# Kernel optimization log

Measured on AMD Instinct MI355X. Metric: run time of the kernel, lower is better.

## Reference

```python
import jax, jax.numpy as jnp
import numpy as np

K = 16          # filter order (number of Laplacian powers)
MLP_OUT = 16    # mlp_hid == mlp_out for mlp_nlayers == 1
D_PE = 64       # phi output dim
BN_EPS = 1e-5
B, N, M = 8, 1024, 128
E = 131072


def setup_inputs() -> dict:
    key = jax.random.key(0)
    ks = jax.random.split(key, 12)
    # Symmetric, spectrally-bounded Laplacian surrogate so 15 matrix powers stay finite.
    A = jax.random.normal(ks[0], (B, N, N), dtype=jnp.float32)
    Lap = (A + jnp.swapaxes(A, -1, -2)) * (0.5 / jnp.sqrt(jnp.float32(N)))
    W = jax.random.normal(ks[1], (B, N, M), dtype=jnp.float32)
    edge_index = jax.random.randint(ks[2], (2, E), 0, B * N, dtype=jnp.int64)
    batch = jnp.repeat(jnp.arange(B, dtype=jnp.int64), N)
    # MLP layer (k -> MLP_OUT) + BatchNorm affine params
    lin_w = jax.random.normal(ks[3], (K, MLP_OUT), dtype=jnp.float32) / jnp.sqrt(jnp.float32(K))
    lin_b = jnp.zeros((MLP_OUT,), dtype=jnp.float32)
    bn_gamma = jnp.ones((MLP_OUT,), dtype=jnp.float32)
    bn_beta = jnp.zeros((MLP_OUT,), dtype=jnp.float32)
    # phi: GIN-style 2-layer MLP after neighbor aggregation
    phi_w1 = jax.random.normal(ks[4], (MLP_OUT, D_PE), dtype=jnp.float32) / jnp.sqrt(jnp.float32(MLP_OUT))
    phi_b1 = jnp.zeros((D_PE,), dtype=jnp.float32)
    phi_w2 = jax.random.normal(ks[5], (D_PE, D_PE), dtype=jnp.float32) / jnp.sqrt(jnp.float32(D_PE))
    phi_b2 = jnp.zeros((D_PE,), dtype=jnp.float32)
    return {"Lap": Lap, "W": W, "lin_w": lin_w, "lin_b": lin_b,
            "bn_gamma": bn_gamma, "bn_beta": bn_beta,
            "phi_w1": phi_w1, "phi_b1": phi_b1, "phi_w2": phi_w2, "phi_b2": phi_b2,
            "edge_index": edge_index, "batch": batch}


def _filter(S, W0):
    """Sequential power filter: returns [k, N, M] = [W0, S@W0, S^2@W0, ...]."""
    def step(out, _):
        nxt = S @ out
        return nxt, nxt
    _, rest = jax.lax.scan(step, W0, None, length=K - 1)
    return jnp.concatenate([W0[None], rest], axis=0)


def reference(Lap, W, lin_w, lin_b, bn_gamma, bn_beta,
              phi_w1, phi_b1, phi_w2, phi_b2, edge_index, batch):
    # Batched filter over all graphs: [B, k, N, M] -> [B, N, M, k]
    feat = jax.vmap(_filter)(Lap, W)
    feat = jnp.transpose(feat, (0, 2, 3, 1))
    # Linear over k -> MLP_OUT channels: [B, N, M, C]
    h = feat @ lin_w + lin_b
    # BatchNorm1d (training mode), per-graph statistics over (N, M) per channel,
    # matching the torch per-graph loop where BN sees [M, C, N].
    mean = jnp.mean(h, axis=(1, 2), keepdims=True)
    var = jnp.var(h, axis=(1, 2), keepdims=True)
    h = (h - mean) * jax.lax.rsqrt(var + BN_EPS) * bn_gamma + bn_beta
    h = jax.nn.relu(h)
    # phi: pool random-sample dim M, flatten graphs -> [N_sum, C]
    x = jnp.mean(h, axis=2).reshape(-1, h.shape[-1])
    src, dst = edge_index[0], edge_index[1]
    agg = jax.ops.segment_sum(x[src], dst, num_segments=x.shape[0])
    g = x + agg  # GIN aggregation
    out = jax.nn.relu(g @ phi_w1 + phi_b1) @ phi_w2 + phi_b2  # [N_sum, D_PE]
    return out
```

## Files before the change

### kernel.cpp

```cpp
#include <hip/hip_runtime.h>

#define B 8
#define N 1024
#define M 128
#define KF 16
#define C 16
#define DPE 64
#define NE 131072
#define NV (B*N)
#define NM (N*M)
#define BN_EPS 1e-5f

typedef short bf16x8 __attribute__((ext_vector_type(8)));
typedef float f32x4 __attribute__((ext_vector_type(4)));

__device__ inline unsigned short f2bf_rne(float f) {
    unsigned u = __float_as_uint(f);
    u += 0x7fffu + ((u >> 16) & 1u);
    return (unsigned short)(u >> 16);
}
__device__ inline float bf2f(unsigned short s) {
    return __uint_as_float((unsigned)s << 16);
}
__device__ inline void split_bf16(float v, unsigned short& hi, unsigned short& lo) {
    hi = f2bf_rne(v);
    float hf = __uint_as_float((unsigned)hi << 16);
    lo = f2bf_rne(v - hf);
}
union U4 { uint4 v; unsigned short s[8]; };
union U2 { uint2 v; unsigned short s[4]; };

__device__ __host__ inline size_t PF4(int b, int msub, int ks, int hl, int l) {
    return ((((size_t)b * 8 + msub) * 32 + ks) * 2 + hl) * 64 + l;
}
#define PFBUF ((size_t)B * 8 * 32 * 2 * 64)

__global__ __launch_bounds__(256) void prep_all(const float* __restrict__ W,
                                                const int* __restrict__ ei,
                                                uint4* __restrict__ Pf,
                                                unsigned short* __restrict__ feat,
                                                int* __restrict__ cnt) {
    __shared__ float T[32][33];
    int blk = blockIdx.x;
    int t = threadIdx.x;
    if (blk < 1024) {
        int b = blk & 7;
        int tile = blk >> 3;
        int nt = tile & 31, mt = tile >> 5;
        int n0 = nt * 32, m0 = mt * 32;
        {
            int nl = t >> 3, mq = t & 7;
            float4 v = *(const float4*)(W + ((size_t)b * N + n0 + nl) * M + m0 + mq * 4);
            T[nl][mq * 4 + 0] = v.x; T[nl][mq * 4 + 1] = v.y;
            T[nl][mq * 4 + 2] = v.z; T[nl][mq * 4 + 3] = v.w;
        }
        __syncthreads();
        {
            int ml = t >> 3, nq = t & 7;
            U2 o;
            o.s[0] = f2bf_rne(T[nq * 4 + 0][ml]);
            o.s[1] = f2bf_rne(T[nq * 4 + 1][ml]);
            o.s[2] = f2bf_rne(T[nq * 4 + 2][ml]);
            o.s[3] = f2bf_rne(T[nq * 4 + 3][ml]);
            unsigned short* plane = feat + (size_t)b * KF * NM;
            *(uint2*)(plane + (size_t)(m0 + ml) * N + n0 + nq * 4) = o.v;
        }
        if (t < 128) {
            int unit = t >> 6, l = t & 63;
            int msub = 2 * mt + unit;
            U4 hi, lo;
            #pragma unroll
            for (int j = 0; j < 8; j++) {
                float v = T[8 * (l >> 4) + j][16 * unit + (l & 15)];
                split_bf16(v, hi.s[j], lo.s[j]);
            }
            Pf[PF4(b, msub, nt, 0, l)] = hi.v;
            Pf[PF4(b, msub, nt, 1, l)] = lo.v;
        }
    } else {
        int e = (blk - 1024) * 256 + t;
        bool is64 = (ei[1] == 0 && ei[3] == 0 && ei[5] == 0 && ei[7] == 0);
        int dst = is64 ? ei[2 * (NE + e)] : ei[NE + e];
        atomicAdd(&cnt[dst], 1);
    }
}

__global__ __launch_bounds__(512) void gemm_chain(const float* __restrict__ Lap,
                                                  uint4* __restrict__ PfA,
                                                  uint4* __restrict__ PfB,
                                                  unsigned short* __restrict__ feat,
                                                  unsigned* bar) {
    extern __shared__ __align__(16) char smem[];
    uint4* ldsS = (uint4*)smem;
    float* Dl = (float*)(smem + 131072);

    int b = blockIdx.x & 7, bx = blockIdx.x >> 3;
    int t = threadIdx.x;
    int w = t >> 6, lane = t & 63;
    int g = w >> 2, wq = w & 3;
    int n0 = 32 * bx;

    {
        int nl = (lane & 15) + 16 * (t >> 8);
        int kg = (lane >> 4) + 4 * ((t >> 6) & 3);
        const float* row = Lap + ((size_t)b * N + n0 + nl) * N;
        int base = (t >> 8) * 4096;
        #pragma unroll
        for (int jj = 0; jj < 8; jj++) {
            int koct = kg + 16 * jj;
            int k0 = koct * 8;
            float4 f0 = *(const float4*)(row + k0);
            float4 f1 = *(const float4*)(row + k0 + 4);
            float e[8] = {f0.x, f0.y, f0.z, f0.w, f1.x, f1.y, f1.z, f1.w};
            U4 hi, lo;
            #pragma unroll
            for (int j = 0; j < 8; j++) split_bf16(e[j], hi.s[j], lo.s[j]);
            int ks = koct >> 2;
            int l = (nl & 15) + 16 * (koct & 3);
            ldsS[base + ks * 128 + l] = hi.v;
            ldsS[base + ks * 128 + 64 + l] = lo.v;
        }
    }
    __syncthreads();

    #pragma unroll 1
    for (int k = 0; k < KF - 1; k++) {
        const uint4* PfIn = (k & 1) ? PfB : PfA;
        uint4* PfOut      = (k & 1) ? PfA : PfB;
        const uint4* Pw0 = PfIn + (size_t)(b * 8 + 2 * wq) * 4096 + (size_t)(16 * g) * 128;
        const uint4* Pw1 = Pw0 + 4096;

        f32x4 acc[2][2] = {};
        uint4 ph[2][2], pl[2][2];
        #pragma unroll
        for (int q = 0; q < 2; q++) {
            ph[q][0] = Pw0[(size_t)q * 128 + lane];
            pl[q][0] = Pw0[(size_t)q * 128 + 64 + lane];
            ph[q][1] = Pw1[(size_t)q * 128 + lane];
            pl[q][1] = Pw1[(size_t)q * 128 + 64 + lane];
        }
        #pragma unroll 2
        for (int ks = 0; ks < 16; ks++) {
            int kg = 16 * g + ks;
            uint4 a0h = ph[ks & 1][0], a0l = pl[ks & 1][0];
            uint4 a1h = ph[ks & 1][1], a1l = pl[ks & 1][1];
            if (ks < 14) {
                ph[ks & 1][0] = Pw0[(size_t)(ks + 2) * 128 + lane];
                pl[ks & 1][0] = Pw0[(size_t)(ks + 2) * 128 + 64 + lane];
                ph[ks & 1][1] = Pw1[(size_t)(ks + 2) * 128 + lane];
                pl[ks & 1][1] = Pw1[(size_t)(ks + 2) * 128 + 64 + lane];
            }
            bf16x8 b0h = __builtin_bit_cast(bf16x8, ldsS[kg * 128 + lane]);
            bf16x8 b0l = __builtin_bit_cast(bf16x8, ldsS[kg * 128 + 64 + lane]);
            bf16x8 b1h = __builtin_bit_cast(bf16x8, ldsS[4096 + kg * 128 + lane]);
            bf16x8 b1l = __builtin_bit_cast(bf16x8, ldsS[4096 + kg * 128 + 64 + lane]);
            bf16x8 A0h = __builtin_bit_cast(bf16x8, a0h);
            bf16x8 A0l = __builtin_bit_cast(bf16x8, a0l);
            bf16x8 A1h = __builtin_bit_cast(bf16x8, a1h);
            bf16x8 A1l = __builtin_bit_cast(bf16x8, a1l);
            acc[0][0] = __builtin_amdgcn_mfma_f32_16x16x32_bf16(A0h, b0h, acc[0][0], 0, 0, 0);
            acc[0][0] = __builtin_amdgcn_mfma_f32_16x16x32_bf16(A0h, b0l, acc[0][0], 0, 0, 0);
            acc[0][0] = __builtin_amdgcn_mfma_f32_16x16x32_bf16(A0l, b0h, acc[0][0], 0, 0, 0);
            acc[0][1] = __builtin_amdgcn_mfma_f32_16x16x32_bf16(A0h, b1h, acc[0][1], 0, 0, 0);
            acc[0][1] = __builtin_amdgcn_mfma_f32_16x16x32_bf16(A0h, b1l, acc[0][1], 0, 0, 0);
            acc[0][1] = __builtin_amdgcn_mfma_f32_16x16x32_bf16(A0l, b1h, acc[0][1], 0, 0, 0);
            acc[1][0] = __builtin_amdgcn_mfma_f32_16x16x32_bf16(A1h, b0h, acc[1][0], 0, 0, 0);
            acc[1][0] = __builtin_amdgcn_mfma_f32_16x16x32_bf16(A1h, b0l, acc[1][0], 0, 0, 0);
            acc[1][0] = __builtin_amdgcn_mfma_f32_16x16x32_bf16(A1l, b0h, acc[1][0], 0, 0, 0);
            acc[1][1] = __builtin_amdgcn_mfma_f32_16x16x32_bf16(A1h, b1h, acc[1][1], 0, 0, 0);
            acc[1][1] = __builtin_amdgcn_mfma_f32_16x16x32_bf16(A1h, b1l, acc[1][1], 0, 0, 0);
            acc[1][1] = __builtin_amdgcn_mfma_f32_16x16x32_bf16(A1l, b1h, acc[1][1], 0, 0, 0);
        }

        if (g == 1) {
            #pragma unroll
            for (int mi = 0; mi < 2; mi++)
                #pragma unroll
                for (int ni = 0; ni < 2; ni++)
                    #pragma unroll
                    for (int r = 0; r < 4; r++) {
                        int m = 32 * wq + 16 * mi + 4 * (lane >> 4) + r;
                        int c = 16 * ni + (lane & 15);
                        Dl[m * 36 + c] = acc[mi][ni][r];
                    }
        }
        __syncthreads();
        if (g == 0) {
            #pragma unroll
            for (int mi = 0; mi < 2; mi++)
                #pragma unroll
                for (int ni = 0; ni < 2; ni++)
                    #pragma unroll
                    for (int r = 0; r < 4; r++) {
                        int m = 32 * wq + 16 * mi + 4 * (lane >> 4) + r;
                        int c = 16 * ni + (lane & 15);
                        Dl[m * 36 + c] += acc[mi][ni][r];
                    }
        }
        __syncthreads();

        {
            int m = t >> 2, c0 = (t & 3) * 8;
            float4 v0 = *(const float4*)&Dl[m * 36 + c0];
            float4 v1 = *(const float4*)&Dl[m * 36 + c0 + 4];
            float e[8] = {v0.x, v0.y, v0.z, v0.w, v1.x, v1.y, v1.z, v1.w};
            U4 hi, lo;
            #pragma unroll
            for (int j = 0; j < 8; j++) split_bf16(e[j], hi.s[j], lo.s[j]);
            unsigned short* plane = feat + ((size_t)b * KF + (k + 1)) * NM
                                        + (size_t)m * N + n0 + c0;
            *(uint4*)plane = hi.v;
            if (k < KF - 2) {
                int l = (m & 15) + 16 * (c0 >> 3);
                PfOut[PF4(b, m >> 4, bx, 0, l)] = hi.v;
                PfOut[PF4(b, m >> 4, bx, 1, l)] = lo.v;
            }
        }
        if (k < KF - 2) {
            __syncthreads();
            if (t == 0) {
                __hip_atomic_fetch_add(&bar[b * 32], 1u, __ATOMIC_RELAXED,
                                       __HIP_MEMORY_SCOPE_AGENT);
                unsigned target = 32u * (unsigned)(k + 1);
                while (__hip_atomic_load(&bar[b * 32], __ATOMIC_RELAXED,
                                         __HIP_MEMORY_SCOPE_AGENT) < target)
                    __builtin_amdgcn_s_sleep(1);
            }
            __syncthreads();
            asm volatile("buffer_inv sc0\n\ts_waitcnt vmcnt(0)" ::: "memory");
        }
    }
}

__global__ __launch_bounds__(256) void bn_stats_scan(const unsigned short* __restrict__ feat,
                                                     const float* __restrict__ lin_w,
                                                     const float* __restrict__ lin_b,
                                                     float* __restrict__ stats,
                                                     const int* __restrict__ cnt,
                                                     int* __restrict__ off,
                                                     int* __restrict__ cur) {
    __shared__ float wls[KF * C];
    __shared__ float red[4][2][C];
    __shared__ int ss[256];
    int t = threadIdx.x;
    if (blockIdx.x < 8) {
        if (blockIdx.x == 0) {
            int base = t * 32;
            int local[32];
            int s = 0;
            #pragma unroll
            for (int i = 0; i < 32; i++) { local[i] = cnt[base + i]; s += local[i]; }
            ss[t] = s;
            __syncthreads();
            #pragma unroll
            for (int d = 1; d < 256; d <<= 1) {
                int v = (t >= d) ? ss[t - d] : 0;
                __syncthreads();
                ss[t] += v;
                __syncthreads();
            }
            int excl = ss[t] - s;
            #pragma unroll
            for (int i = 0; i < 32; i++) { off[base + i] = excl; cur[base + i] = excl; excl += local[i]; }
        }
        return;
    }
    int blk = blockIdx.x - 8;
    wls[t] = lin_w[t];
    __syncthreads();
    int b = blk & 7;
    int i = (blk >> 3) * 256 + t;
    const uint2* fb = (const uint2*)(feat + (size_t)b * KF * NM);

    float4 hacc[C];
    #pragma unroll
    for (int c = 0; c < C; c++) {
        float bb = lin_b[c];
        hacc[c] = make_float4(bb, bb, bb, bb);
    }
    for (int kk = 0; kk < KF; kk++) {
        U2 u; u.v = fb[(size_t)kk * (NM / 4) + i];
        float p0 = bf2f(u.s[0]), p1 = bf2f(u.s[1]), p2 = bf2f(u.s[2]), p3 = bf2f(u.s[3]);
        #pragma unroll
        for (int c = 0; c < C; c++) {
            float wv = wls[kk * C + c];
            hacc[c].x = fmaf(p0, wv, hacc[c].x);
            hacc[c].y = fmaf(p1, wv, hacc[c].y);
            hacc[c].z = fmaf(p2, wv, hacc[c].z);
            hacc[c].w = fmaf(p3, wv, hacc[c].w);
        }
    }
    float s[C], ssq[C];
    #pragma unroll
    for (int c = 0; c < C; c++) {
        float4 hh = hacc[c];
        s[c] = hh.x + hh.y + hh.z + hh.w;
        ssq[c] = hh.x * hh.x + hh.y * hh.y + hh.z * hh.z + hh.w * hh.w;
    }
    #pragma unroll
    for (int o = 32; o > 0; o >>= 1)
        #pragma unroll
        for (int c = 0; c < C; c++) {
            s[c] += __shfl_down(s[c], o);
            ssq[c] += __shfl_down(ssq[c], o);
        }
    if ((t & 63) == 0) {
        int wv = t >> 6;
        #pragma unroll
        for (int c = 0; c < C; c++) { red[wv][0][c] = s[c]; red[wv][1][c] = ssq[c]; }
    }
    __syncthreads();
    if (t < 32) {
        int which = t >> 4, c = t & 15;
        float v = red[0][which][c] + red[1][which][c] + red[2][which][c] + red[3][which][c];
        atomicAdd(&stats[b * 32 + which * 16 + c], v);
    }
}

__global__ __launch_bounds__(256) void bnx_fill(const unsigned short* __restrict__ feat,
                                                const float* __restrict__ lin_w,
                                                const float* __restrict__ lin_b,
                                                const float* __restrict__ gam,
                                                const float* __restrict__ bet,
                                                const float* __restrict__ stats,
                                                float* __restrict__ x,
                                                const int* __restrict__ ei,
                                                int* __restrict__ cur,
                                                int* __restrict__ bucket) {
    __shared__ float wls[KF * C];
    __shared__ float red[8][32 * 17];
    int t = threadIdx.x;
    if (blockIdx.x >= 256) {
        int e = (blockIdx.x - 256) * 256 + t;
        bool is64 = (ei[1] == 0 && ei[3] == 0 && ei[5] == 0 && ei[7] == 0);
        int src, dst;
        if (is64) { src = ei[2 * e]; dst = ei[2 * (NE + e)]; }
        else      { src = ei[e];     dst = ei[NE + e]; }
        int pos = atomicAdd(&cur[dst], 1);
        bucket[pos] = src;
        return;
    }
    wls[t] = lin_w[t];
    __syncthreads();
    int grp = blockIdx.x;
    int b = grp & 7, n0 = (grp >> 3) * 32;
    int nl = t & 31, mg = t >> 5;
    int n = n0 + nl;

    const float inv_nm = 1.0f / (float)NM;
    float sc[C], sh[C], bb[C];
    #pragma unroll
    for (int c = 0; c < C; c++) {
        float mean = stats[b * 32 + c] * inv_nm;
        float var = stats[b * 32 + 16 + c] * inv_nm - mean * mean;
        sc[c] = gam[c] * rsqrtf(var + BN_EPS);
        sh[c] = bet[c] - mean * sc[c];
        bb[c] = lin_b[c];
    }
    const unsigned short* fb = feat + (size_t)b * KF * NM + n;
    float y[C] = {};
    for (int m = mg * 16; m < mg * 16 + 16; m++) {
        float p[KF];
        #pragma unroll
        for (int kk = 0; kk < KF; kk++) p[kk] = bf2f(fb[(size_t)kk * NM + (size_t)m * N]);
        #pragma unroll
        for (int c = 0; c < C; c++) {
            float hh = bb[c];
            #pragma unroll
            for (int kk = 0; kk < KF; kk++) hh = fmaf(p[kk], wls[kk * C + c], hh);
            y[c] += fmaxf(fmaf(hh, sc[c], sh[c]), 0.0f);
        }
    }
    #pragma unroll
    for (int c = 0; c < C; c++) red[mg][nl * 17 + c] = y[c];
    __syncthreads();
    #pragma unroll
    for (int q = 0; q < 2; q++) {
        int slot = t + q * 256;
        int snl = slot >> 4, c = slot & 15;
        float v = 0.0f;
        #pragma unroll
        for (int m8 = 0; m8 < 8; m8++) v += red[m8][snl * 17 + c];
        v *= (1.0f / (float)M);
        x[((size_t)b * N + n0 + snl) * C + c] = v;
    }
}

__global__ __launch_bounds__(256) void phi_fused(const int* __restrict__ cnt,
                                                 const int* __restrict__ off,
                                                 const int* __restrict__ bucket,
                                                 const float* __restrict__ x,
                                                 const float* __restrict__ w1,
                                                 const float* __restrict__ b1,
                                                 const float* __restrict__ w2,
                                                 const float* __restrict__ b2,
                                                 float* __restrict__ out) {
    __shared__ float w1s[C * DPE];
    __shared__ float w2s[DPE * DPE];
    __shared__ float b2s[DPE];
    __shared__ float gsh[16][17];
    __shared__ float h1sh[16][DPE];
    int t = threadIdx.x;
    #pragma unroll
    for (int q = 0; q < 4; q++) w1s[t + q * 256] = w1[t + q * 256];
    #pragma unroll
    for (int q = 0; q < 16; q++) w2s[t + q * 256] = w2[t + q * 256];
    if (t < DPE) b2s[t] = b2[t];

    {
        int nl = t >> 4, c = t & 15;
        int n = blockIdx.x * 16 + nl;
        int o = off[n], d = cnt[n];
        float v = x[(size_t)n * C + c];
        int j = 0;
        for (; j + 4 <= d; j += 4) {
            int s0 = bucket[o + j], s1 = bucket[o + j + 1];
            int s2 = bucket[o + j + 2], s3 = bucket[o + j + 3];
            v += x[(size_t)s0 * C + c];
            v += x[(size_t)s1 * C + c];
            v += x[(size_t)s2 * C + c];
            v += x[(size_t)s3 * C + c];
        }
        for (; j < d; j++) v += x[(size_t)bucket[o + j] * C + c];
        gsh[nl][c] = v;
    }
    __syncthreads();
    #pragma unroll
    for (int q = 0; q < 4; q++) {
        int item = t + 256 * q;
        int node = item >> 6, j = item & 63;
        float h = b1[j];
        #pragma unroll
        for (int c = 0; c < C; c++) h = fmaf(gsh[node][c], w1s[c * DPE + j], h);
        h1sh[node][j] = fmaxf(h, 0.0f);
    }
    __syncthreads();
    #pragma unroll
    for (int q = 0; q < 4; q++) {
        int item = t + 256 * q;
        int node = item >> 6, d = item & 63;
        float o2 = b2s[d];
        #pragma unroll
        for (int j = 0; j < DPE; j++) o2 = fmaf(h1sh[node][j], w2s[j * DPE + d], o2);
        out[((size_t)blockIdx.x * 16 + node) * DPE + d] = o2;
    }
}

extern "C" void kernel_launch(void* const* d_in, const int* in_sizes, int n_in,
                              void* d_out, int out_size, void* d_ws, size_t ws_size,
                              hipStream_t stream) {
    const float* Lap   = (const float*)d_in[0];
    const float* W     = (const float*)d_in[1];
    const float* lin_w = (const float*)d_in[2];
    const float* lin_b = (const float*)d_in[3];
    const float* gam   = (const float*)d_in[4];
    const float* bet   = (const float*)d_in[5];
    const float* w1    = (const float*)d_in[6];
    const float* b1    = (const float*)d_in[7];
    const float* w2    = (const float*)d_in[8];
    const float* b2    = (const float*)d_in[9];
    const int*   ei    = (const int*)d_in[10];

    char* wsb = (char*)d_ws;
    unsigned short* feat = (unsigned short*)wsb;
    uint4* Pf    = (uint4*)(wsb + ((size_t)32 << 20));
    char* tail   = wsb + ((size_t)40 << 20);
    float* stats = (float*)tail;
    unsigned* bar = (unsigned*)(tail + 1024);
    int* cnt     = (int*)(tail + 8192);
    float* x     = (float*)(tail + 40960);
    int* off     = (int*)(x + (size_t)NV * C);
    int* cur     = off + NV;
    int* bucket  = cur + NV;
    float* out   = (float*)d_out;

    static bool attr_set = false;
    if (!attr_set) {
        hipFuncSetAttribute((const void*)gemm_chain,
                            hipFuncAttributeMaxDynamicSharedMemorySize, 149504);
        attr_set = true;
    }

    hipMemsetAsync(tail, 0, 40960, stream);
    prep_all<<<dim3(1536), 256, 0, stream>>>(W, ei, Pf, feat, cnt);
    gemm_chain<<<dim3(256), 512, 149504, stream>>>(Lap, Pf, Pf + PFBUF, feat, bar);
    bn_stats_scan<<<dim3(1032), 256, 0, stream>>>(feat, lin_w, lin_b, stats, cnt, off, cur);
    bnx_fill<<<dim3(768), 256, 0, stream>>>(feat, lin_w, lin_b, gam, bet, stats, x, ei, cur, bucket);
    phi_fused<<<dim3(NV / 16), 256, 0, stream>>>(cnt, off, bucket, x, w1, b1, w2, b2, out);
}
```

Baseline: 274.7 us.

## Fuse BN statistics and normalize-pool into one kernel with grid barrier

Merges the BatchNorm statistics pass and the normalize/ReLU/mean-pool pass into one kernel. Each block stages its 32-node feature tile in LDS once, computes partial stats, waits on a per-graph spin barrier, then reuses the LDS tile for the second pass. This avoids reading the bf16 feature tensor from global memory twice. The edge-bucket fill moves to its own kernel. The spin barrier relies on all 257 blocks being co-resident, and the large LDS footprint allows only one block per CU.

Result: slower. 304.8 us (+10.9%).

```diff
diff --git a/kernel.cpp b/kernel.cpp
--- a/kernel.cpp
+++ b/kernel.cpp
@@ -232,158 +232,170 @@
     }
 }
 
-__global__ __launch_bounds__(256) void bn_stats_scan(const unsigned short* __restrict__ feat,
-                                                     const float* __restrict__ lin_w,
-                                                     const float* __restrict__ lin_b,
-                                                     float* __restrict__ stats,
-                                                     const int* __restrict__ cnt,
-                                                     int* __restrict__ off,
-                                                     int* __restrict__ cur) {
-    __shared__ float wls[KF * C];
-    __shared__ float red[4][2][C];
-    __shared__ int ss[256];
-    int t = threadIdx.x;
-    if (blockIdx.x < 8) {
-        if (blockIdx.x == 0) {
-            int base = t * 32;
-            int local[32];
-            int s = 0;
-            #pragma unroll
-            for (int i = 0; i < 32; i++) { local[i] = cnt[base + i]; s += local[i]; }
-            ss[t] = s;
-            __syncthreads();
-            #pragma unroll
-            for (int d = 1; d < 256; d <<= 1) {
-                int v = (t >= d) ? ss[t - d] : 0;
-                __syncthreads();
-                ss[t] += v;
-                __syncthreads();
-            }
-            int excl = ss[t] - s;
-            #pragma unroll
-            for (int i = 0; i < 32; i++) { off[base + i] = excl; cur[base + i] = excl; excl += local[i]; }
-        }
-        return;
-    }
-    int blk = blockIdx.x - 8;
-    wls[t] = lin_w[t];
-    __syncthreads();
-    int b = blk & 7;
-    int i = (blk >> 3) * 256 + t;
-    const uint2* fb = (const uint2*)(feat + (size_t)b * KF * NM);
-
-    float4 hacc[C];
-    #pragma unroll
-    for (int c = 0; c < C; c++) {
-        float bb = lin_b[c];
-        hacc[c] = make_float4(bb, bb, bb, bb);
-    }
-    for (int kk = 0; kk < KF; kk++) {
-        U2 u; u.v = fb[(size_t)kk * (NM / 4) + i];
-        float p0 = bf2f(u.s[0]), p1 = bf2f(u.s[1]), p2 = bf2f(u.s[2]), p3 = bf2f(u.s[3]);
-        #pragma unroll
-        for (int c = 0; c < C; c++) {
-            float wv = wls[kk * C + c];
-            hacc[c].x = fmaf(p0, wv, hacc[c].x);
-            hacc[c].y = fmaf(p1, wv, hacc[c].y);
-            hacc[c].z = fmaf(p2, wv, hacc[c].z);
-            hacc[c].w = fmaf(p3, wv, hacc[c].w);
-        }
-    }
-    float s[C], ssq[C];
-    #pragma unroll
-    for (int c = 0; c < C; c++) {
-        float4 hh = hacc[c];
-        s[c] = hh.x + hh.y + hh.z + hh.w;
-        ssq[c] = hh.x * hh.x + hh.y * hh.y + hh.z * hh.z + hh.w * hh.w;
-    }
-    #pragma unroll
-    for (int o = 32; o > 0; o >>= 1)
-        #pragma unroll
-        for (int c = 0; c < C; c++) {
-            s[c] += __shfl_down(s[c], o);
-            ssq[c] += __shfl_down(ssq[c], o);
-        }
-    if ((t & 63) == 0) {
-        int wv = t >> 6;
-        #pragma unroll
-        for (int c = 0; c < C; c++) { red[wv][0][c] = s[c]; red[wv][1][c] = ssq[c]; }
-    }
-    __syncthreads();
-    if (t < 32) {
-        int which = t >> 4, c = t & 15;
-        float v = red[0][which][c] + red[1][which][c] + red[2][which][c] + red[3][which][c];
-        atomicAdd(&stats[b * 32 + which * 16 + c], v);
-    }
-}
-
-__global__ __launch_bounds__(256) void bnx_fill(const unsigned short* __restrict__ feat,
+#define KSTR 4112
+__global__ __launch_bounds__(512) void bn_fused(const unsigned short* __restrict__ feat,
                                                 const float* __restrict__ lin_w,
                                                 const float* __restrict__ lin_b,
                                                 const float* __restrict__ gam,
                                                 const float* __restrict__ bet,
-                                                const float* __restrict__ stats,
+                                                float* __restrict__ stats,
+                                                unsigned* bar,
                                                 float* __restrict__ x,
-                                                const int* __restrict__ ei,
-                                                int* __restrict__ cur,
-                                                int* __restrict__ bucket) {
+                                                const int* __restrict__ cnt,
+                                                int* __restrict__ off,
+                                                int* __restrict__ cur) {
+    extern __shared__ __align__(16) char smem2[];
+    unsigned short* fs = (unsigned short*)smem2;
+    float* red = (float*)(smem2 + 131584);
     __shared__ float wls[KF * C];
-    __shared__ float red[8][32 * 17];
+    __shared__ int ss[256];
     int t = threadIdx.x;
+
     if (blockIdx.x >= 256) {
-        int e = (blockIdx.x - 256) * 256 + t;
-        bool is64 = (ei[1] == 0 && ei[3] == 0 && ei[5] == 0 && ei[7] == 0);
-        int src, dst;
-        if (is64) { src = ei[2 * e]; dst = ei[2 * (NE + e)]; }
-        else      { src = ei[e];     dst = ei[NE + e]; }
-        int pos = atomicAdd(&cur[dst], 1);
-        bucket[pos] = src;
+        int s = 0;
+        int local[32];
+        int base = t * 32;
+        if (t < 256) {
+            #pragma unroll
+            for (int i = 0; i < 32; i++) { local[i] = cnt[base + i]; s += local[i]; }
+            ss[t] = s;
+        }
+        __syncthreads();
+        #pragma unroll
+        for (int d = 1; d < 256; d <<= 1) {
+            int v = (t >= d && t < 256) ? ss[t - d] : 0;
+            __syncthreads();
+            if (t < 256) ss[t] += v;
+            __syncthreads();
+        }
+        if (t < 256) {
+            int excl = ss[t] - s;
+            #pragma unroll
+            for (int i = 0; i < 32; i++) { off[base + i] = excl; cur[base + i] = excl; excl += local[i]; }
+        }
         return;
     }
-    wls[t] = lin_w[t];
-    __syncthreads();
-    int grp = blockIdx.x;
-    int b = grp & 7, n0 = (grp >> 3) * 32;
-    int nl = t & 31, mg = t >> 5;
-    int n = n0 + nl;
+
+    int b = blockIdx.x & 7, n0 = (blockIdx.x >> 3) * 32;
+    if (t < KF * C) wls[t] = lin_w[t];
+
+    uint4* fsu = (uint4*)fs;
+    #pragma unroll
+    for (int i = 0; i < 16; i++) {
+        int idx = t + 512 * i;
+        int k = idx >> 9, r = idx & 511;
+        int m = r >> 2, c = r & 3;
+        const uint4* src = (const uint4*)(feat + ((size_t)b * KF + k) * NM
+                                               + (size_t)m * N + n0);
+        fsu[k * (KSTR / 8) + m * 4 + c] = src[c];
+    }
+    __syncthreads();
+
+    float bb[C];
+    #pragma unroll
+    for (int c = 0; c < C; c++) bb[c] = lin_b[c];
+    float s[C] = {}, ssq[C] = {};
+    #pragma unroll
+    for (int j = 0; j < 8; j++) {
+        int e = t + 512 * j;
+        float p[KF];
+        #pragma unroll
+        for (int kk = 0; kk < KF; kk++) p[kk] = bf2f(fs[kk * KSTR + e]);
+        #pragma unroll
+        for (int c = 0; c < C; c++) {
+            float h = bb[c];
+            #pragma unroll
+            for (int kk = 0; kk < KF; kk++) h = fmaf(p[kk], wls[kk * C + c], h);
+            s[c] += h;
+            ssq[c] = fmaf(h, h, ssq[c]);
+        }
+    }
+    #pragma unroll
+    for (int o = 32; o > 0; o >>= 1)
+        #pragma unroll
+        for (int c = 0; c < C; c++) {
+            s[c] += __shfl_down(s[c], o);
+            ssq[c] += __shfl_down(ssq[c], o);
+        }
+    int w = t >> 6;
+    if ((t & 63) == 0) {
+        #pragma unroll
+        for (int c = 0; c < C; c++) { red[w * 32 + c] = s[c]; red[256 + w * 32 + c] = ssq[c]; }
+    }
+    __syncthreads();
+    if (t < 32) {
+        int which = t >> 4, c = t & 15;
+        float v = 0.0f;
+        #pragma unroll
+        for (int wv = 0; wv < 8; wv++) v += red[which * 256 + wv * 32 + c];
+        atomicAdd(&stats[b * 32 + which * 16 + c], v);
+    }
+    __syncthreads();
+
+    if (t == 0) {
+        __hip_atomic_fetch_add(&bar[256 + b * 32], 1u, __ATOMIC_RELAXED,
+                               __HIP_MEMORY_SCOPE_AGENT);
+        while (__hip_atomic_load(&bar[256 + b * 32], __ATOMIC_RELAXED,
+                                 __HIP_MEMORY_SCOPE_AGENT) < 32u)
+            __builtin_amdgcn_s_sleep(1);
+    }
+    __syncthreads();
+    asm volatile("buffer_inv sc0\n\ts_waitcnt vmcnt(0)" ::: "memory");
 
     const float inv_nm = 1.0f / (float)NM;
-    float sc[C], sh[C], bb[C];
+    float sc[C], sh[C];
     #pragma unroll
     for (int c = 0; c < C; c++) {
         float mean = stats[b * 32 + c] * inv_nm;
         float var = stats[b * 32 + 16 + c] * inv_nm - mean * mean;
         sc[c] = gam[c] * rsqrtf(var + BN_EPS);
         sh[c] = bet[c] - mean * sc[c];
-        bb[c] = lin_b[c];
-    }
-    const unsigned short* fb = feat + (size_t)b * KF * NM + n;
+    }
+    int nl = t & 31, mg = t >> 5;
     float y[C] = {};
-    for (int m = mg * 16; m < mg * 16 + 16; m++) {
+    #pragma unroll
+    for (int mi = 0; mi < 8; mi++) {
+        int m = mg * 8 + mi;
         float p[KF];
         #pragma unroll
-        for (int kk = 0; kk < KF; kk++) p[kk] = bf2f(fb[(size_t)kk * NM + (size_t)m * N]);
+        for (int kk = 0; kk < KF; kk++) p[kk] = bf2f(fs[kk * KSTR + m * 32 + nl]);
         #pragma unroll
         for (int c = 0; c < C; c++) {
-            float hh = bb[c];
-            #pragma unroll
-            for (int kk = 0; kk < KF; kk++) hh = fmaf(p[kk], wls[kk * C + c], hh);
-            y[c] += fmaxf(fmaf(hh, sc[c], sh[c]), 0.0f);
-        }
-    }
-    #pragma unroll
-    for (int c = 0; c < C; c++) red[mg][nl * 17 + c] = y[c];
-    __syncthreads();
-    #pragma unroll
-    for (int q = 0; q < 2; q++) {
-        int slot = t + q * 256;
-        int snl = slot >> 4, c = slot & 15;
+            float h = bb[c];
+            #pragma unroll
+            for (int kk = 0; kk < KF; kk++) h = fmaf(p[kk], wls[kk * C + c], h);
+            y[c] += fmaxf(fmaf(h, sc[c], sh[c]), 0.0f);
+        }
+    }
+    if (mg < 8) {
+        #pragma unroll
+        for (int c = 0; c < C; c++) red[mg * 544 + nl * 17 + c] = y[c];
+    }
+    __syncthreads();
+    if (mg >= 8) {
+        #pragma unroll
+        for (int c = 0; c < C; c++) red[(mg - 8) * 544 + nl * 17 + c] += y[c];
+    }
+    __syncthreads();
+    {
+        int snl = t >> 4, c = t & 15;
         float v = 0.0f;
         #pragma unroll
-        for (int m8 = 0; m8 < 8; m8++) v += red[m8][snl * 17 + c];
-        v *= (1.0f / (float)M);
-        x[((size_t)b * N + n0 + snl) * C + c] = v;
-    }
+        for (int m8 = 0; m8 < 8; m8++) v += red[m8 * 544 + snl * 17 + c];
+        x[((size_t)b * N + n0 + snl) * C + c] = v * (1.0f / (float)M);
+    }
+}
+
+__global__ __launch_bounds__(256) void edge_fill(const int* __restrict__ ei,
+                                                 int* __restrict__ cur,
+                                                 int* __restrict__ bucket) {
+    int e = blockIdx.x * 256 + threadIdx.x;
+    bool is64 = (ei[1] == 0 && ei[3] == 0 && ei[5] == 0 && ei[7] == 0);
+    int src, dst;
+    if (is64) { src = ei[2 * e]; dst = ei[2 * (NE + e)]; }
+    else      { src = ei[e];     dst = ei[NE + e]; }
+    int pos = atomicAdd(&cur[dst], 1);
+    bucket[pos] = src;
 }
 
 __global__ __launch_bounds__(256) void phi_fused(const int* __restrict__ cnt,
@@ -478,13 +490,16 @@
     if (!attr_set) {
         hipFuncSetAttribute((const void*)gemm_chain,
                             hipFuncAttributeMaxDynamicSharedMemorySize, 149504);
+        hipFuncSetAttribute((const void*)bn_fused,
+                            hipFuncAttributeMaxDynamicSharedMemorySize, 148992);
         attr_set = true;
     }
 
     hipMemsetAsync(tail, 0, 40960, stream);
     prep_all<<<dim3(1536), 256, 0, stream>>>(W, ei, Pf, feat, cnt);
     gemm_chain<<<dim3(256), 512, 149504, stream>>>(Lap, Pf, Pf + PFBUF, feat, bar);
-    bn_stats_scan<<<dim3(1032), 256, 0, stream>>>(feat, lin_w, lin_b, stats, cnt, off, cur);
-    bnx_fill<<<dim3(768), 256, 0, stream>>>(feat, lin_w, lin_b, gam, bet, stats, x, ei, cur, bucket);
+    bn_fused<<<dim3(257), 512, 148992, stream>>>(feat, lin_w, lin_b, gam, bet,
+                                                 stats, bar, x, cnt, off, cur);
+    edge_fill<<<dim3(NE / 256), 256, 0, stream>>>(ei, cur, bucket);
     phi_fused<<<dim3(NV / 16), 256, 0, stream>>>(cnt, off, bucket, x, w1, b1, w2, b2, out);
 }
```

## Fuse W preparation and edge counting into the GEMM chain kernel

Applied to the files above, without the earlier changes.

Removes the separate prep_all kernel. Each gemm_chain block now loads its own 32-row W tile into LDS, splits it into bf16 hi/lo panels, writes the first feature plane, and counts in-degrees for 512 edges. A per-graph global counter barrier then makes sure all 32 blocks of that graph have written their panels before the power chain starts. This saves one kernel launch and one global round trip. The cost is an extra cross-block spin barrier and cache invalidate at the start of the chain, which relies on all 256 blocks being resident at once.

Result: no change. 275.2 us (+0.2%).

```diff
diff --git a/kernel.cpp b/kernel.cpp
--- a/kernel.cpp
+++ b/kernel.cpp
@@ -35,61 +35,14 @@
 }
 #define PFBUF ((size_t)B * 8 * 32 * 2 * 64)
 
-__global__ __launch_bounds__(256) void prep_all(const float* __restrict__ W,
-                                                const int* __restrict__ ei,
-                                                uint4* __restrict__ Pf,
-                                                unsigned short* __restrict__ feat,
-                                                int* __restrict__ cnt) {
-    __shared__ float T[32][33];
-    int blk = blockIdx.x;
-    int t = threadIdx.x;
-    if (blk < 1024) {
-        int b = blk & 7;
-        int tile = blk >> 3;
-        int nt = tile & 31, mt = tile >> 5;
-        int n0 = nt * 32, m0 = mt * 32;
-        {
-            int nl = t >> 3, mq = t & 7;
-            float4 v = *(const float4*)(W + ((size_t)b * N + n0 + nl) * M + m0 + mq * 4);
-            T[nl][mq * 4 + 0] = v.x; T[nl][mq * 4 + 1] = v.y;
-            T[nl][mq * 4 + 2] = v.z; T[nl][mq * 4 + 3] = v.w;
-        }
-        __syncthreads();
-        {
-            int ml = t >> 3, nq = t & 7;
-            U2 o;
-            o.s[0] = f2bf_rne(T[nq * 4 + 0][ml]);
-            o.s[1] = f2bf_rne(T[nq * 4 + 1][ml]);
-            o.s[2] = f2bf_rne(T[nq * 4 + 2][ml]);
-            o.s[3] = f2bf_rne(T[nq * 4 + 3][ml]);
-            unsigned short* plane = feat + (size_t)b * KF * NM;
-            *(uint2*)(plane + (size_t)(m0 + ml) * N + n0 + nq * 4) = o.v;
-        }
-        if (t < 128) {
-            int unit = t >> 6, l = t & 63;
-            int msub = 2 * mt + unit;
-            U4 hi, lo;
-            #pragma unroll
-            for (int j = 0; j < 8; j++) {
-                float v = T[8 * (l >> 4) + j][16 * unit + (l & 15)];
-                split_bf16(v, hi.s[j], lo.s[j]);
-            }
-            Pf[PF4(b, msub, nt, 0, l)] = hi.v;
-            Pf[PF4(b, msub, nt, 1, l)] = lo.v;
-        }
-    } else {
-        int e = (blk - 1024) * 256 + t;
-        bool is64 = (ei[1] == 0 && ei[3] == 0 && ei[5] == 0 && ei[7] == 0);
-        int dst = is64 ? ei[2 * (NE + e)] : ei[NE + e];
-        atomicAdd(&cnt[dst], 1);
-    }
-}
-
 __global__ __launch_bounds__(512) void gemm_chain(const float* __restrict__ Lap,
+                                                  const float* __restrict__ W,
+                                                  const int* __restrict__ ei,
                                                   uint4* __restrict__ PfA,
                                                   uint4* __restrict__ PfB,
                                                   unsigned short* __restrict__ feat,
-                                                  unsigned* bar) {
+                                                  unsigned* bar,
+                                                  int* __restrict__ cnt) {
     extern __shared__ __align__(16) char smem[];
     uint4* ldsS = (uint4*)smem;
     float* Dl = (float*)(smem + 131072);
@@ -121,7 +74,48 @@
             ldsS[base + ks * 128 + 64 + l] = lo.v;
         }
     }
-    __syncthreads();
+    {
+        const float4* wsrc = (const float4*)(W + ((size_t)b * N + n0) * M);
+        float4* dl4 = (float4*)Dl;
+        dl4[t] = wsrc[t];
+        dl4[t + 512] = wsrc[t + 512];
+    }
+    __syncthreads();
+
+    {
+        int msub = t >> 6, l = lane;
+        U4 hi, lo;
+        #pragma unroll
+        for (int j = 0; j < 8; j++) {
+            float v = Dl[(8 * (l >> 4) + j) * 128 + 16 * msub + (l & 15)];
+            split_bf16(v, hi.s[j], lo.s[j]);
+        }
+        PfA[PF4(b, msub, bx, 0, l)] = hi.v;
+        PfA[PF4(b, msub, bx, 1, l)] = lo.v;
+        __syncthreads();
+        if (t == 0)
+            __hip_atomic_fetch_add(&bar[256 + b * 32], 1u, __ATOMIC_RELAXED,
+                                   __HIP_MEMORY_SCOPE_AGENT);
+        {
+            int m = 16 * msub + (l & 15);
+            unsigned short* plane = feat + (size_t)b * KF * NM
+                                        + (size_t)m * N + n0 + 8 * (l >> 4);
+            *(uint4*)plane = hi.v;
+        }
+        {
+            int e = blockIdx.x * 512 + t;
+            bool is64 = (ei[1] == 0 && ei[3] == 0 && ei[5] == 0 && ei[7] == 0);
+            int dst = is64 ? ei[2 * (NE + e)] : ei[NE + e];
+            atomicAdd(&cnt[dst], 1);
+        }
+        if (t == 0) {
+            while (__hip_atomic_load(&bar[256 + b * 32], __ATOMIC_RELAXED,
+                                     __HIP_MEMORY_SCOPE_AGENT) < 32u)
+                __builtin_amdgcn_s_sleep(1);
+        }
+        __syncthreads();
+        asm volatile("buffer_inv sc0\n\ts_waitcnt vmcnt(0)" ::: "memory");
+    }
 
     #pragma unroll 1
     for (int k = 0; k < KF - 1; k++) {
@@ -482,8 +476,8 @@
     }
 
     hipMemsetAsync(tail, 0, 40960, stream);
-    prep_all<<<dim3(1536), 256, 0, stream>>>(W, ei, Pf, feat, cnt);
-    gemm_chain<<<dim3(256), 512, 149504, stream>>>(Lap, Pf, Pf + PFBUF, feat, bar);
+    gemm_chain<<<dim3(256), 512, 149504, stream>>>(Lap, W, ei, Pf, Pf + PFBUF,
+                                                   feat, bar, cnt);
     bn_stats_scan<<<dim3(1032), 256, 0, stream>>>(feat, lin_w, lin_b, stats, cnt, off, cur);
     bnx_fill<<<dim3(768), 256, 0, stream>>>(feat, lin_w, lin_b, gam, bet, stats, x, ei, cur, bucket);
     phi_fused<<<dim3(NV / 16), 256, 0, stream>>>(cnt, off, bucket, x, w1, b1, w2, b2, out);
```
